# Kernel optimization log

Hardware: AMD Instinct MI355X
Metric: run time of the kernel (lower is better)

The kernel has to match this reference:

```python
import jax, jax.numpy as jnp
import numpy as np

B, D, H, DH, L = 2, 1024, 16, 64, 4
FF = 4 * D
COUNTS = (512, 256, 128, 64, 16)  # seq, local_seq, scattering, expression, fusion
EPS = 1e-5


def layer_norm(x, gamma):
    mu = jnp.mean(x, axis=-1, keepdims=True)
    var = jnp.mean((x - mu) ** 2, axis=-1, keepdims=True)
    return (x - mu) * jax.lax.rsqrt(var + EPS) * gamma


def build_zorro_mask(counts):
    # faithful to the torch code, including the `|` / `==` precedence quirk:
    # zorro_mask_fusion = (zorro_mask | tf) == FUSION(4)
    types = jnp.concatenate([jnp.full((c,), i, dtype=jnp.int32) for i, c in enumerate(counts)])
    tf, tt = types[:, None], types[None, :]
    m0 = tf == tt
    fusion_rows = (m0.astype(jnp.int32) | tf) == 4
    mask = m0 | fusion_rows
    S = int(sum(counts))
    nf = counts[4]
    exp_rows = (types == 3)[:, None]
    col_ok = (jnp.arange(S) < (S - nf))[None, :]
    return mask | (exp_rows & col_ok)


def setup_inputs() -> dict:
    key = jax.random.key(0)
    ks = jax.random.split(key, 13)
    s = 0.02
    inp = {
        "rna_tokens": jax.random.normal(ks[0], (B, COUNTS[0], D), jnp.float32),
        "roi_tokens": jax.random.normal(ks[1], (B, COUNTS[1], D), jnp.float32),
        "structure_tokens": jax.random.normal(ks[2], (B, COUNTS[2], D), jnp.float32),
        "expression_tokens": jax.random.normal(ks[3], (B, COUNTS[3], D), jnp.float32),
        "fusion_tokens": jax.random.normal(ks[4], (B, COUNTS[4], D), jnp.float32),
        "qw": jax.random.normal(ks[5], (L, D, H * DH), jnp.float32) * s,
        "kvw": jax.random.normal(ks[6], (L, D, 2 * H * DH), jnp.float32) * s,
        "ow": jax.random.normal(ks[7], (L, H * DH, D), jnp.float32) * s,
        "ag": jnp.ones((L, D), jnp.float32),
        "fg": jnp.ones((L, D), jnp.float32),
        "w1": jax.random.normal(ks[8], (L, D, FF), jnp.float32) * s,
        "w2": jax.random.normal(ks[9], (L, FF, D), jnp.float32) * s,
        "gamma": jnp.ones((D,), jnp.float32),
    }
    return inp


def reference(rna_tokens, roi_tokens, structure_tokens, expression_tokens, fusion_tokens,
              qw, kvw, ow, ag, fg, w1, w2, gamma):
    streams = (rna_tokens, roi_tokens, structure_tokens, expression_tokens, fusion_tokens)
    counts = tuple(t.shape[1] for t in streams)
    tokens = jnp.concatenate(streams, axis=1)  # [B, S, D]
    b, S, d = tokens.shape
    mask = build_zorro_mask(counts)  # [S, S] bool
    scale = DH ** -0.5
    neg = jnp.finfo(tokens.dtype).min
    attn_list = []
    for l in range(L):
        x = layer_norm(tokens, ag[l])
        q = (x @ qw[l]).reshape(b, S, H, DH)
        kv = x @ kvw[l]
        k = kv[..., : H * DH].reshape(b, S, H, DH)
        v = kv[..., H * DH:].reshape(b, S, H, DH)
        sim = jnp.einsum('bihd,bjhd->bhij', q, k) * scale
        sim = jnp.where(mask, sim, neg)
        attn = jax.nn.softmax(sim, axis=-1)  # [B, H, S, S]
        attn_list.append(attn)
        out = jnp.einsum('bhij,bjhd->bihd', attn, v).reshape(b, S, H * DH) @ ow[l]
        tokens = out + tokens
        y = layer_norm(tokens, fg[l])
        tokens = jax.nn.gelu(y @ w1[l], approximate=False) @ w2[l] + tokens
    tokens = layer_norm(tokens, gamma)
    splits = np.cumsum(counts)[:-1].tolist()
    seq_t, local_t, scat_t, exp_t, fus_t = jnp.split(tokens, splits, axis=1)
    return (seq_t, local_t, scat_t, exp_t, fus_t, jnp.stack(attn_list))
```

## Files before the change

kernel.cpp:

```cpp
#include <hip/hip_runtime.h>
#include <math.h>
#include <stdint.h>

typedef __bf16 bf16;
typedef __attribute__((ext_vector_type(8))) bf16 bf16x8;
typedef __attribute__((ext_vector_type(4))) bf16 bf16x4;
typedef __attribute__((ext_vector_type(4))) float f4;

__device__ __forceinline__ f4 mfma(bf16x8 a, bf16x8 b, f4 c){
  return __builtin_amdgcn_mfma_f32_16x16x32_bf16(a, b, c, 0, 0, 0);
}

static constexpr int S_TOT = 976;
static constexpr int MR = 1952;
static constexpr int MRP = 2048;
static constexpr size_t ATT_BASE = 1998848;
static constexpr size_t ATT_L = 30482432;

__device__ __forceinline__ void gload16(const void* g, const void* l){
  __builtin_amdgcn_global_load_lds(
      (const __attribute__((address_space(1))) void*)(uintptr_t)g,
      (__attribute__((address_space(3))) void*)(uint32_t)(uintptr_t)l,
      16, 0, 0);
}

__device__ __forceinline__ unsigned pk2(float a, float b){
  unsigned short ua = __builtin_bit_cast(unsigned short, (bf16)a);
  unsigned short ub = __builtin_bit_cast(unsigned short, (bf16)b);
  return ((unsigned)ub << 16) | (unsigned)ua;
}

__global__ __launch_bounds__(256) void k_concat_ln(const float* __restrict__ r0, const float* __restrict__ r1,
                                                   const float* __restrict__ r2, const float* __restrict__ r3,
                                                   const float* __restrict__ r4, const float* __restrict__ g,
                                                   float* __restrict__ tok, bf16* __restrict__ xb){
  int wid = threadIdx.x >> 6, lane = threadIdx.x & 63;
  int row = blockIdx.x*4 + wid;
  int b = row / S_TOT, s = row % S_TOT;
  const float* src; int off;
  if (s < 512)      { src = r0; off = b*512 + s; }
  else if (s < 768) { src = r1; off = b*256 + (s-512); }
  else if (s < 896) { src = r2; off = b*128 + (s-768); }
  else if (s < 960) { src = r3; off = b*64  + (s-896); }
  else              { src = r4; off = b*16  + (s-960); }
  const f4* p = (const f4*)src + (size_t)off*256;
  f4 v[4];
  float sum=0.f, sq=0.f;
#pragma unroll
  for (int i=0;i<4;i++){
    v[i] = p[i*64 + lane];
    ((f4*)(tok + (size_t)row*1024))[i*64 + lane] = v[i];
#pragma unroll
    for (int c=0;c<4;c++){ float x=v[i][c]; sum+=x; sq+=x*x; }
  }
#pragma unroll
  for (int d=1; d<64; d<<=1){ sum += __shfl_xor(sum,d); sq += __shfl_xor(sq,d); }
  float mu = sum*(1.f/1024.f);
  float var = sq*(1.f/1024.f) - mu*mu;
  float rs = rsqrtf(var + 1e-5f);
#pragma unroll
  for (int i=0;i<4;i++){
    f4 gg = ((const f4*)g)[i*64 + lane];
    bf16x4 o;
#pragma unroll
    for (int c=0;c<4;c++) o[c] = (bf16)((v[i][c]-mu)*rs*gg[c]);
    *(bf16x4*)&xb[(size_t)row*1024 + (size_t)(i*64+lane)*4] = o;
  }
}

__global__ __launch_bounds__(256) void k_ln_bf(const float* __restrict__ in, const float* __restrict__ g,
                                               bf16* __restrict__ out){
  int wid = threadIdx.x >> 6, lane = threadIdx.x & 63;
  int row = blockIdx.x*4 + wid;
  const float* p = in + (size_t)row*1024;
  f4 v[4];
#pragma unroll
  for (int i=0;i<4;i++) v[i] = ((const f4*)p)[i*64 + lane];
  float sum=0.f, sq=0.f;
#pragma unroll
  for (int i=0;i<4;i++){
#pragma unroll
    for (int c=0;c<4;c++){ float x=v[i][c]; sum+=x; sq+=x*x; } }
#pragma unroll
  for (int d=1; d<64; d<<=1){ sum += __shfl_xor(sum,d); sq += __shfl_xor(sq,d); }
  float mu = sum*(1.f/1024.f);
  float var = sq*(1.f/1024.f) - mu*mu;
  float rs = rsqrtf(var + 1e-5f);
#pragma unroll
  for (int i=0;i<4;i++){
    f4 gg = ((const f4*)g)[i*64 + lane];
    bf16x4 o;
#pragma unroll
    for (int c=0;c<4;c++) o[c] = (bf16)((v[i][c]-mu)*rs*gg[c]);
    *(bf16x4*)&out[(size_t)row*1024 + (size_t)(i*64+lane)*4] = o;
  }
}

template<bool LN>
__global__ __launch_bounds__(256) void k_red_ln(const float* __restrict__ pA, float* __restrict__ tokens,
                                                const float* __restrict__ g, bf16* __restrict__ xb){
  int wid = threadIdx.x >> 6, lane = threadIdx.x & 63;
  int row = blockIdx.x*4 + wid;
  const float* p0 = pA + (size_t)row*1024;
  const float* p1 = pA + (size_t)MRP*1024 + (size_t)row*1024;
  float* tp = tokens + (size_t)row*1024;
  f4 v[4];
  float sum=0.f, sq=0.f;
#pragma unroll
  for (int i=0;i<4;i++){
    f4 a = ((const f4*)p0)[i*64 + lane];
    f4 b = ((const f4*)p1)[i*64 + lane];
    f4 t = ((const f4*)tp)[i*64 + lane];
#pragma unroll
    for (int c=0;c<4;c++){ float x = t[c] + a[c] + b[c]; v[i][c] = x; if (LN){ sum += x; sq += x*x; } }
    ((f4*)tp)[i*64 + lane] = v[i];
  }
  if (LN){
#pragma unroll
    for (int d=1; d<64; d<<=1){ sum += __shfl_xor(sum,d); sq += __shfl_xor(sq,d); }
    float mu = sum*(1.f/1024.f);
    float var = sq*(1.f/1024.f) - mu*mu;
    float rs = rsqrtf(var + 1e-5f);
#pragma unroll
    for (int i=0;i<4;i++){
      f4 gg = ((const f4*)g)[i*64 + lane];
      bf16x4 o;
#pragma unroll
      for (int c=0;c<4;c++) o[c] = (bf16)((v[i][c]-mu)*rs*gg[c]);
      *(bf16x4*)&xb[(size_t)row*1024 + (size_t)(i*64+lane)*4] = o;
    }
  }
}

__global__ __launch_bounds__(256) void k_red_ln_out(const float* __restrict__ pA, float* __restrict__ tokens,
                                                    const float* __restrict__ g, float* __restrict__ out){
  int wid = threadIdx.x >> 6, lane = threadIdx.x & 63;
  int row = blockIdx.x*4 + wid;
  int b = row / S_TOT, s = row % S_TOT;
  size_t dst;
  if (s < 512)      dst = (size_t)(b*512 + s)*1024;
  else if (s < 768) dst = 1048576 + (size_t)(b*256 + (s-512))*1024;
  else if (s < 896) dst = 1572864 + (size_t)(b*128 + (s-768))*1024;
  else if (s < 960) dst = 1835008 + (size_t)(b*64  + (s-896))*1024;
  else              dst = 1966080 + (size_t)(b*16  + (s-960))*1024;
  const float* p0 = pA + (size_t)row*1024;
  const float* p1 = pA + (size_t)MRP*1024 + (size_t)row*1024;
  const float* tp = tokens + (size_t)row*1024;
  f4 v[4];
  float sum=0.f, sq=0.f;
#pragma unroll
  for (int i=0;i<4;i++){
    f4 a = ((const f4*)p0)[i*64 + lane];
    f4 bb = ((const f4*)p1)[i*64 + lane];
    f4 t = ((const f4*)tp)[i*64 + lane];
#pragma unroll
    for (int c=0;c<4;c++){ float x = t[c] + a[c] + bb[c]; v[i][c] = x; sum += x; sq += x*x; }
  }
#pragma unroll
  for (int d=1; d<64; d<<=1){ sum += __shfl_xor(sum,d); sq += __shfl_xor(sq,d); }
  float mu = sum*(1.f/1024.f);
  float var = sq*(1.f/1024.f) - mu*mu;
  float rs = rsqrtf(var + 1e-5f);
#pragma unroll
  for (int i=0;i<4;i++){
    f4 gg = ((const f4*)g)[i*64 + lane];
    f4 o;
#pragma unroll
    for (int c=0;c<4;c++) o[c] = (v[i][c]-mu)*rs*gg[c];
    ((f4*)(out + dst))[i*64 + lane] = o;
  }
}

__global__ __launch_bounds__(256) void k_wtransz(const float* __restrict__ src, int ldsrc, int coloff, long srcZ,
                                                 bf16* __restrict__ dst, int K, long dstZ){
  src += (size_t)blockIdx.z*srcZ;
  dst += (size_t)blockIdx.z*dstZ;
  __shared__ float t[32][33];
  int kb = blockIdx.x*32, nb = blockIdx.y*32;
  int tx = threadIdx.x & 31, ty = threadIdx.x >> 5;
#pragma unroll
  for (int i=0;i<32;i+=8) t[ty+i][tx] = src[(size_t)(kb+ty+i)*ldsrc + coloff + nb + tx];
  __syncthreads();
#pragma unroll
  for (int i=0;i<32;i+=8) dst[(size_t)(nb+ty+i)*K + kb + tx] = (bf16)t[tx][ty+i];
}

__global__ __launch_bounds__(256) void k_attn_pv(const bf16* __restrict__ q, const bf16* __restrict__ k,
                                                 const bf16* __restrict__ vT, int ld,
                                                 float* __restrict__ aout, bf16* __restrict__ O){
  int z = blockIdx.y; int b = z >> 4, h = z & 15;
  int wid = threadIdx.x >> 6, lane = threadIdx.x & 63;
  int r0 = (blockIdx.x*4 + wid)*16;
  if (r0 >= S_TOT) return;
  int cs, ce;
  if (r0 < 512)      { cs = 0;   ce = 512; }
  else if (r0 < 768) { cs = 512; ce = 768; }
  else if (r0 < 896) { cs = 768; ce = 896; }
  else if (r0 < 960) { cs = 0;   ce = 960; }
  else               { cs = 0;   ce = 976; }
  int lm = lane & 15, lg = lane >> 4;
  const float scale = 0.125f;
  const bf16* qp = q + (size_t)(b*S_TOT + r0 + lm)*ld + h*64 + lg*8;
  bf16x8 qf0 = *(const bf16x8*)qp;
  bf16x8 qf1 = *(const bf16x8*)(qp + 32);
  const bf16* kbase = k + (size_t)b*S_TOT*ld + h*64 + lg*8;
  const bf16* vbase = vT + (size_t)z*64*S_TOT;
  int nfull = (ce - cs) & ~31;
  bool tail = ((ce - cs) & 16) != 0;
  float s = 0.f;
  for (int cb = cs; cb < cs + nfull; cb += 32){
    const bf16* kp = kbase + (size_t)(cb + lm)*ld;
    bf16x8 k00 = *(const bf16x8*)kp;
    bf16x8 k01 = *(const bf16x8*)(kp + 32);
    const bf16* kp2 = kp + (size_t)16*ld;
    bf16x8 k10 = *(const bf16x8*)kp2;
    bf16x8 k11 = *(const bf16x8*)(kp2 + 32);
    f4 c0 = {0.f,0.f,0.f,0.f}, c1 = {0.f,0.f,0.f,0.f};
    __builtin_amdgcn_s_setprio(1);
    c0 = mfma(k00, qf0, c0); c0 = mfma(k01, qf1, c0);
    c1 = mfma(k10, qf0, c1); c1 = mfma(k11, qf1, c1);
    __builtin_amdgcn_s_setprio(0);
#pragma unroll
    for (int r=0;r<4;r++) s += __expf(c0[r]*scale) + __expf(c1[r]*scale);
  }
  if (tail){
    int cb = cs + nfull;
    const bf16* kp = kbase + (size_t)(cb + lm)*ld;
    bf16x8 k00 = *(const bf16x8*)kp;
    bf16x8 k01 = *(const bf16x8*)(kp + 32);
    f4 c0 = {0.f,0.f,0.f,0.f};
    c0 = mfma(k00, qf0, c0); c0 = mfma(k01, qf1, c0);
#pragma unroll
    for (int r=0;r<4;r++) s += __expf(c0[r]*scale);
  }
  s += __shfl_xor(s, 16);
  s += __shfl_xor(s, 32);
  float inv = 1.f / s;
  float* orow = aout + (size_t)z*S_TOT*S_TOT + (size_t)(r0 + lm)*S_TOT;
  f4 acc[4];
#pragma unroll
  for (int nf=0;nf<4;nf++){ f4 zf = {0.f,0.f,0.f,0.f}; acc[nf] = zf; }
  bool msel = (lg >= 2);
  int srcA = lm + ((lg & 1) << 5);
  int srcB = srcA + 16;
  auto step = [&](int cb, bool has2){
    const bf16* kp = kbase + (size_t)(cb + lm)*ld;
    bf16x8 k00 = *(const bf16x8*)kp;
    bf16x8 k01 = *(const bf16x8*)(kp + 32);
    f4 c0 = {0.f,0.f,0.f,0.f}, c1 = {0.f,0.f,0.f,0.f};
    __builtin_amdgcn_s_setprio(1);
    c0 = mfma(k00, qf0, c0); c0 = mfma(k01, qf1, c0);
    if (has2){
      const bf16* kp2 = kp + (size_t)16*ld;
      bf16x8 k10 = *(const bf16x8*)kp2;
      bf16x8 k11 = *(const bf16x8*)(kp2 + 32);
      c1 = mfma(k10, qf0, c1); c1 = mfma(k11, qf1, c1);
    }
    __builtin_amdgcn_s_setprio(0);
    f4 p0, p1;
#pragma unroll
    for (int r=0;r<4;r++) p0[r] = __expf(c0[r]*scale)*inv;
#pragma unroll
    for (int r=0;r<4;r++) p1[r] = has2 ? __expf(c1[r]*scale)*inv : 0.f;
    *(f4*)(orow + cb + lg*4) = p0;
    if (has2) *(f4*)(orow + cb + 16 + lg*4) = p1;
    unsigned lo0 = pk2(p0[0], p0[1]), hi0 = pk2(p0[2], p0[3]);
    unsigned lo1 = pk2(p1[0], p1[1]), hi1 = pk2(p1[2], p1[3]);
    unsigned a0 = __shfl(lo0, srcA), a1 = __shfl(lo1, srcA);
    unsigned b0 = __shfl(hi0, srcA), b1 = __shfl(hi1, srcA);
    unsigned c0s = __shfl(lo0, srcB), c1s = __shfl(lo1, srcB);
    unsigned d0 = __shfl(hi0, srcB), d1 = __shfl(hi1, srcB);
    union { unsigned u[4]; bf16x8 v; } pu;
    pu.u[0] = msel ? a1 : a0;
    pu.u[1] = msel ? b1 : b0;
    pu.u[2] = msel ? c1s : c0s;
    pu.u[3] = msel ? d1 : d0;
    bf16x8 pa = pu.v;
    __builtin_amdgcn_s_setprio(1);
#pragma unroll
    for (int nf=0;nf<4;nf++){
      bf16x8 vf = *(const bf16x8*)(vbase + (size_t)(nf*16 + lm)*S_TOT + cb + lg*8);
      acc[nf] = mfma(pa, vf, acc[nf]);
    }
    __builtin_amdgcn_s_setprio(0);
  };
  for (int cb = cs; cb < cs + nfull; cb += 32) step(cb, true);
  if (tail) step(cs + nfull, false);
  bf16* obase = O + (size_t)(b*S_TOT + r0)*1024 + h*64;
#pragma unroll
  for (int nf=0;nf<4;nf++)
#pragma unroll
    for (int r=0;r<4;r++)
      obase[(size_t)(lg*4 + r)*1024 + nf*16 + lm] = (bf16)acc[nf][r];
  float* zrow = aout + (size_t)z*S_TOT*S_TOT + (size_t)r0*S_TOT;
  int cs4 = cs >> 2, ce4 = ce >> 2;
  for (int r2=0;r2<16;r2++){
    f4* rb = (f4*)(zrow + (size_t)r2*S_TOT);
    f4 zf = {0.f,0.f,0.f,0.f};
    for (int c4 = lane; c4 < cs4; c4 += 64)        rb[c4] = zf;
    for (int c4 = ce4 + lane; c4 < 244; c4 += 64)  rb[c4] = zf;
  }
}

template<int BM, bool OUTBF, bool RESID, bool GELU, bool VT>
__global__ __launch_bounds__(256) void k_gemm2(
    const bf16* __restrict__ A, int lda,
    const bf16* __restrict__ Bw, int ldb,
    float* __restrict__ Cf, bf16* __restrict__ Cb, int ldc,
    const float* __restrict__ R, bf16* __restrict__ vTout,
    int M, int N, int K, int kz, long cz)
{
  constexpr int MF = BM/32;
  __shared__ bf16 As[2][BM*32];
  __shared__ bf16 Bs[2][128*32];
  int tid = threadIdx.x, lane = tid & 63, wid = tid >> 6;
  int lm = lane & 15, lg = lane >> 4;
  int wr = (wid >> 1)*(BM/2), wc = (wid & 1)*64;
  int mb = blockIdx.x*BM, nb = blockIdx.y*128;
  int bz = blockIdx.z;
  f4 acc[MF][4];
#pragma unroll
  for (int i=0;i<MF;i++)
#pragma unroll
    for (int j=0;j<4;j++){ f4 zf = {0.f,0.f,0.f,0.f}; acc[i][j] = zf; }
  const bf16* Ab = A + (size_t)mb*lda + (size_t)bz*kz;
  const bf16* Bb = Bw + (size_t)nb*ldb + (size_t)bz*kz;
  auto stage = [&](int kt, int buf){
    int k0 = kt*32;
#pragma unroll
    for (int it=0; it<BM/64; it++){
      int cb = it*256 + wid*64;
      int c  = cb + lane;
      gload16(Ab + (size_t)(c>>2)*lda + k0 + (c&3)*8, (char*)As[buf] + cb*16);
    }
#pragma unroll
    for (int it=0; it<2; it++){
      int cb = it*256 + wid*64;
      int c  = cb + lane;
      gload16(Bb + (size_t)(c>>2)*ldb + k0 + (c&3)*8, (char*)Bs[buf] + cb*16);
    }
  };
  stage(0, 0);
  __syncthreads();
  int nkt = K/32;
  for (int kt=0; kt<nkt; kt++){
    int cur = kt & 1;
    if (kt+1 < nkt) stage(kt+1, cur^1);
    bf16x8 af[MF], bfr[4];
#pragma unroll
    for (int mf=0; mf<MF; mf++) af[mf] = *(bf16x8*)&As[cur][(wr + mf*16 + lm)*32 + lg*8];
#pragma unroll
    for (int nf=0; nf<4; nf++)  bfr[nf] = *(bf16x8*)&Bs[cur][(wc + nf*16 + lm)*32 + lg*8];
#pragma unroll
    for (int mf=0; mf<MF; mf++)
#pragma unroll
      for (int nf=0; nf<4; nf++)
        acc[mf][nf] = mfma(af[mf], bfr[nf], acc[mf][nf]);
    __syncthreads();
  }
#pragma unroll
  for (int mf=0; mf<MF; mf++)
#pragma unroll
    for (int nf=0; nf<4; nf++)
#pragma unroll
      for (int r=0; r<4; r++){
        int row = mb + wr + mf*16 + lg*4 + r;
        if (row < M){
          int col = nb + wc + nf*16 + lm;
          float vv = acc[mf][nf][r];
          if (RESID) vv += R[(size_t)row*ldc + col];
          if (GELU){
            float u2 = vv*(1.5957691216f + 0.0713548162f*vv*vv);
            float e = __expf(u2);
            vv = vv - vv/(e + 1.f);
          }
          if (OUTBF) Cb[(size_t)row*ldc + col] = (bf16)vv;
          else       Cf[(size_t)bz*cz + (size_t)row*ldc + col] = vv;
        }
      }
  if constexpr (VT){
    if (nb >= 2048){
      __shared__ __align__(16) bf16 Ts[128][72];
#pragma unroll
      for (int hb=0; hb<2; hb++){
        __syncthreads();
        if ((wid >> 1) == hb){
#pragma unroll
          for (int mf=0; mf<MF; mf++)
#pragma unroll
            for (int nf=0; nf<4; nf++)
#pragma unroll
              for (int r=0; r<4; r++)
                Ts[wc + nf*16 + lm][mf*16 + lg*4 + r] = (bf16)acc[mf][nf][r];
        }
        __syncthreads();
        int dc = tid >> 1;
        int rh = (tid & 1)*32;
#pragma unroll
        for (int j=0;j<4;j++){
          int lr = rh + j*8;
          int srow = mb + hb*64 + lr;
          if (srow < MR){
            int bb = srow >= S_TOT;
            int ss = srow - bb*S_TOT;
            int gn = nb - 2048 + dc;
            bf16x8 d = *(bf16x8*)&Ts[dc][lr];
            *(bf16x8*)&vTout[((size_t)(bb*16 + (gn>>6))*64 + (gn&63))*S_TOT + ss] = d;
          }
        }
      }
    }
  }
}

extern "C" void kernel_launch(void* const* d_in, const int* in_sizes, int n_in,
                              void* d_out, int out_size, void* d_ws, size_t ws_size,
                              hipStream_t stream) {
  const float* rna  = (const float*)d_in[0];
  const float* roi  = (const float*)d_in[1];
  const float* stru = (const float*)d_in[2];
  const float* expr = (const float*)d_in[3];
  const float* fus  = (const float*)d_in[4];
  const float* qw   = (const float*)d_in[5];
  const float* kvw  = (const float*)d_in[6];
  const float* ow   = (const float*)d_in[7];
  const float* ag   = (const float*)d_in[8];
  const float* fg   = (const float*)d_in[9];
  const float* w1   = (const float*)d_in[10];
  const float* w2   = (const float*)d_in[11];
  const float* gamma= (const float*)d_in[12];
  float* out = (float*)d_out;

  char* wsb = (char*)d_ws;
  size_t off = 0;
  auto alc = [&](size_t n)->char*{ char* p = wsb + off; off = (off + n + 255) & ~(size_t)255; return p; };
  float* tokens = (float*)alc((size_t)MRP*1024*4);
  float* pA    = (float*)alc((size_t)2*MRP*1024*4);
  bf16* xb    = (bf16*)alc((size_t)MRP*1024*2);
  bf16* qkv   = (bf16*)alc((size_t)MRP*3072*2);
  bf16* vT    = (bf16*)alc((size_t)32*64*S_TOT*2);
  bf16* attno = (bf16*)alc((size_t)MRP*1024*2);
  bf16* hb    = (bf16*)alc((size_t)MRP*4096*2);
  bf16* wqkvT = (bf16*)alc((size_t)4*3072*1024*2);
  bf16* woT   = (bf16*)alc((size_t)4*1024*1024*2);
  bf16* w1T   = (bf16*)alc((size_t)4*4096*1024*2);
  bf16* w2T   = (bf16*)alc((size_t)4*4096*1024*2);
  if (off > ws_size) return;

  k_wtransz<<<dim3(32,32,4),  256, 0, stream>>>(qw,  1024, 0,    1048576, wqkvT,             1024, 3145728);
  k_wtransz<<<dim3(32,32,4),  256, 0, stream>>>(kvw, 2048, 0,    2097152, wqkvT + 1024*1024, 1024, 3145728);
  k_wtransz<<<dim3(32,32,4),  256, 0, stream>>>(kvw, 2048, 1024, 2097152, wqkvT + 2048*1024, 1024, 3145728);
  k_wtransz<<<dim3(32,32,4),  256, 0, stream>>>(ow,  1024, 0,    1048576, woT, 1024, 1048576);
  k_wtransz<<<dim3(32,128,4), 256, 0, stream>>>(w1,  4096, 0,    4194304, w1T, 1024, 4194304);
  k_wtransz<<<dim3(128,32,4), 256, 0, stream>>>(w2,  1024, 0,    4194304, w2T, 4096, 4194304);

  k_concat_ln<<<MR/4, 256, 0, stream>>>(rna, roi, stru, expr, fus, ag, tokens, xb);

  for (int l=0; l<4; l++){
    k_gemm2<128,true,false,false,true><<<dim3(16,24), 256, 0, stream>>>(
        xb, 1024, wqkvT + (size_t)l*3145728, 1024, nullptr, qkv, 3072, nullptr, vT, MR, 3072, 1024, 0, 0);

    float* attL = out + ATT_BASE + (size_t)l*ATT_L;
    k_attn_pv<<<dim3(16,32), 256, 0, stream>>>(qkv, qkv + 1024, vT, 3072, attL, attno);

    k_gemm2<64,false,true,false,false><<<dim3(31,8), 256, 0, stream>>>(
        attno, 1024, woT + (size_t)l*1048576, 1024, tokens, nullptr, 1024, tokens, nullptr, MR, 1024, 1024, 0, 0);

    k_ln_bf<<<MR/4, 256, 0, stream>>>(tokens, fg + l*1024, xb);

    k_gemm2<128,true,false,true,false><<<dim3(16,32), 256, 0, stream>>>(
        xb, 1024, w1T + (size_t)l*4194304, 1024, nullptr, hb, 4096, nullptr, nullptr, MR, 4096, 1024, 0, 0);

    k_gemm2<128,false,false,false,false><<<dim3(16,8,2), 256, 0, stream>>>(
        hb, 4096, w2T + (size_t)l*4194304, 4096, pA, nullptr, 1024, nullptr, nullptr, MR, 1024, 2048,
        2048, (long)MRP*1024);

    if (l < 3) k_red_ln<true><<<MR/4, 256, 0, stream>>>(pA, tokens, ag + (l+1)*1024, xb);
    else       k_red_ln_out<<<MR/4, 256, 0, stream>>>(pA, tokens, gamma, out);
  }
}
```

Baseline: 1.022 ms.

## Switch GEMM to 32x32x16 MFMA and swizzle block order for XCD locality

The GEMM kernel now uses the 32x32x16 bf16 MFMA instruction instead of 16x16x32. This halves the LDS fragment loads per MFMA and should raise matrix-core throughput. Both the GEMM and attention kernels also remap the linear block index so that consecutive blocks land on chiplets in groups of eight, which aims to improve L2 reuse across XCDs. The remap assumes the grid size is divisible by 8; if it is not, some tiles could be skipped or duplicated.

```diff
diff --git a/kernel.cpp b/kernel.cpp
--- a/kernel.cpp
+++ b/kernel.cpp
@@ -6,9 +6,13 @@
 typedef __attribute__((ext_vector_type(8))) bf16 bf16x8;
 typedef __attribute__((ext_vector_type(4))) bf16 bf16x4;
 typedef __attribute__((ext_vector_type(4))) float f4;
+typedef __attribute__((ext_vector_type(16))) float f16v;
 
 __device__ __forceinline__ f4 mfma(bf16x8 a, bf16x8 b, f4 c){
   return __builtin_amdgcn_mfma_f32_16x16x32_bf16(a, b, c, 0, 0, 0);
+}
+__device__ __forceinline__ f16v mfma32(bf16x8 a, bf16x8 b, f16v c){
+  return __builtin_amdgcn_mfma_f32_32x32x16_bf16(a, b, c, 0, 0, 0);
 }
 
 static constexpr int S_TOT = 976;
@@ -188,9 +192,14 @@
 __global__ __launch_bounds__(256) void k_attn_pv(const bf16* __restrict__ q, const bf16* __restrict__ k,
                                                  const bf16* __restrict__ vT, int ld,
                                                  float* __restrict__ aout, bf16* __restrict__ O){
-  int z = blockIdx.y; int b = z >> 4, h = z & 15;
+  int nxy = gridDim.x * gridDim.y;
+  int lin0 = blockIdx.y * gridDim.x + blockIdx.x;
+  int lin = (lin0 & 7)*(nxy >> 3) + (lin0 >> 3);
+  int bxs = lin % gridDim.x;
+  int z = lin / gridDim.x;
+  int b = z >> 4, h = z & 15;
   int wid = threadIdx.x >> 6, lane = threadIdx.x & 63;
-  int r0 = (blockIdx.x*4 + wid)*16;
+  int r0 = (bxs*4 + wid)*16;
   if (r0 >= S_TOT) return;
   int cs, ce;
   if (r0 < 512)      { cs = 0;   ce = 512; }
@@ -310,19 +319,24 @@
     const float* __restrict__ R, bf16* __restrict__ vTout,
     int M, int N, int K, int kz, long cz)
 {
-  constexpr int MF = BM/32;
+  constexpr int MI = BM/64;
   __shared__ bf16 As[2][BM*32];
   __shared__ bf16 Bs[2][128*32];
   int tid = threadIdx.x, lane = tid & 63, wid = tid >> 6;
-  int lm = lane & 15, lg = lane >> 4;
+  int l31 = lane & 31, kh = lane >> 5;
   int wr = (wid >> 1)*(BM/2), wc = (wid & 1)*64;
-  int mb = blockIdx.x*BM, nb = blockIdx.y*128;
+  int nxy = gridDim.x * gridDim.y;
+  int lin0 = blockIdx.y * gridDim.x + blockIdx.x;
+  int lin = (lin0 & 7)*(nxy >> 3) + (lin0 >> 3);
+  int mb = (lin % gridDim.x)*BM, nb = (lin / gridDim.x)*128;
   int bz = blockIdx.z;
-  f4 acc[MF][4];
-#pragma unroll
-  for (int i=0;i<MF;i++)
-#pragma unroll
-    for (int j=0;j<4;j++){ f4 zf = {0.f,0.f,0.f,0.f}; acc[i][j] = zf; }
+  f16v acc[MI][2];
+#pragma unroll
+  for (int i=0;i<MI;i++)
+#pragma unroll
+    for (int j=0;j<2;j++)
+#pragma unroll
+      for (int e=0;e<16;e++) acc[i][j][e] = 0.f;
   const bf16* Ab = A + (size_t)mb*lda + (size_t)bz*kz;
   const bf16* Bb = Bw + (size_t)nb*ldb + (size_t)bz*kz;
   auto stage = [&](int kt, int buf){
@@ -346,28 +360,36 @@
   for (int kt=0; kt<nkt; kt++){
     int cur = kt & 1;
     if (kt+1 < nkt) stage(kt+1, cur^1);
-    bf16x8 af[MF], bfr[4];
-#pragma unroll
-    for (int mf=0; mf<MF; mf++) af[mf] = *(bf16x8*)&As[cur][(wr + mf*16 + lm)*32 + lg*8];
-#pragma unroll
-    for (int nf=0; nf<4; nf++)  bfr[nf] = *(bf16x8*)&Bs[cur][(wc + nf*16 + lm)*32 + lg*8];
-#pragma unroll
-    for (int mf=0; mf<MF; mf++)
-#pragma unroll
-      for (int nf=0; nf<4; nf++)
-        acc[mf][nf] = mfma(af[mf], bfr[nf], acc[mf][nf]);
+    bf16x8 af[MI][2], bfr[2][2];
+#pragma unroll
+    for (int mi=0; mi<MI; mi++)
+#pragma unroll
+      for (int ks=0; ks<2; ks++)
+        af[mi][ks] = *(bf16x8*)&As[cur][(wr + mi*32 + l31)*32 + ks*16 + kh*8];
+#pragma unroll
+    for (int ni=0; ni<2; ni++)
+#pragma unroll
+      for (int ks=0; ks<2; ks++)
+        bfr[ni][ks] = *(bf16x8*)&Bs[cur][(wc + ni*32 + l31)*32 + ks*16 + kh*8];
+#pragma unroll
+    for (int mi=0; mi<MI; mi++)
+#pragma unroll
+      for (int ni=0; ni<2; ni++)
+#pragma unroll
+        for (int ks=0; ks<2; ks++)
+          acc[mi][ni] = mfma32(af[mi][ks], bfr[ni][ks], acc[mi][ni]);
     __syncthreads();
   }
 #pragma unroll
-  for (int mf=0; mf<MF; mf++)
-#pragma unroll
-    for (int nf=0; nf<4; nf++)
-#pragma unroll
-      for (int r=0; r<4; r++){
-        int row = mb + wr + mf*16 + lg*4 + r;
+  for (int mi=0; mi<MI; mi++)
+#pragma unroll
+    for (int ni=0; ni<2; ni++){
+      int col = nb + wc + ni*32 + l31;
+#pragma unroll
+      for (int reg=0; reg<16; reg++){
+        int row = mb + wr + mi*32 + (reg&3) + 8*(reg>>2) + 4*kh;
         if (row < M){
-          int col = nb + wc + nf*16 + lm;
-          float vv = acc[mf][nf][r];
+          float vv = acc[mi][ni][reg];
           if (RESID) vv += R[(size_t)row*ldc + col];
           if (GELU){
             float u2 = vv*(1.5957691216f + 0.0713548162f*vv*vv);
@@ -378,6 +400,7 @@
           else       Cf[(size_t)bz*cz + (size_t)row*ldc + col] = vv;
         }
       }
+    }
   if constexpr (VT){
     if (nb >= 2048){
       __shared__ __align__(16) bf16 Ts[128][72];
@@ -386,12 +409,12 @@
         __syncthreads();
         if ((wid >> 1) == hb){
 #pragma unroll
-          for (int mf=0; mf<MF; mf++)
-#pragma unroll
-            for (int nf=0; nf<4; nf++)
-#pragma unroll
-              for (int r=0; r<4; r++)
-                Ts[wc + nf*16 + lm][mf*16 + lg*4 + r] = (bf16)acc[mf][nf][r];
+          for (int mi=0; mi<MI; mi++)
+#pragma unroll
+            for (int ni=0; ni<2; ni++)
+#pragma unroll
+              for (int reg=0; reg<16; reg++)
+                Ts[wc + ni*32 + l31][mi*32 + (reg&3) + 8*(reg>>2) + 4*kh] = (bf16)acc[mi][ni][reg];
         }
         __syncthreads();
         int dc = tid >> 1;
```

Result: slower. 1.054 ms (+3.2%).

## Merge weight transposes into one launch and hoist attention mask zeroing

Applied to the files above, without the earlier changes.

Replaces the six weight-transpose launches with a single kernel that decodes which matrix and tile each block handles. It also moves the zero-fill of masked attention-probability entries out of the per-layer attention kernel into one upfront kernel covering all four layers, using 256 threads per block. This is meant to cut launch overhead and take the zero-store tail off the attention kernel's critical path. The cost is one large separate zero-fill pass over the attention output at the start.

```diff
diff --git a/kernel.cpp b/kernel.cpp
--- a/kernel.cpp
+++ b/kernel.cpp
@@ -28,6 +28,29 @@
   unsigned short ua = __builtin_bit_cast(unsigned short, (bf16)a);
   unsigned short ub = __builtin_bit_cast(unsigned short, (bf16)b);
   return ((unsigned)ub << 16) | (unsigned)ua;
+}
+
+__device__ __forceinline__ void mask_span(int r0, int& cs, int& ce){
+  if (r0 < 512)      { cs = 0;   ce = 512; }
+  else if (r0 < 768) { cs = 512; ce = 768; }
+  else if (r0 < 896) { cs = 768; ce = 896; }
+  else if (r0 < 960) { cs = 0;   ce = 960; }
+  else               { cs = 0;   ce = 976; }
+}
+
+__global__ __launch_bounds__(256) void k_zero_mask(float* __restrict__ aout){
+  int z = blockIdx.y;
+  int r0 = blockIdx.x*16;
+  float* base = aout + (size_t)blockIdx.z*ATT_L + (size_t)z*S_TOT*S_TOT;
+  int cs, ce; mask_span(r0, cs, ce);
+  int cs4 = cs >> 2, ce4 = ce >> 2;
+  f4 zf = {0.f,0.f,0.f,0.f};
+#pragma unroll
+  for (int r2=0;r2<16;r2++){
+    f4* rb = (f4*)(base + (size_t)(r0 + r2)*S_TOT);
+    for (int c4 = threadIdx.x; c4 < cs4; c4 += 256)        rb[c4] = zf;
+    for (int c4 = ce4 + threadIdx.x; c4 < 244; c4 += 256)  rb[c4] = zf;
+  }
 }
 
 __global__ __launch_bounds__(256) void k_concat_ln(const float* __restrict__ r0, const float* __restrict__ r1,
@@ -171,18 +194,43 @@
   }
 }
 
-__global__ __launch_bounds__(256) void k_wtransz(const float* __restrict__ src, int ldsrc, int coloff, long srcZ,
-                                                 bf16* __restrict__ dst, int K, long dstZ){
-  src += (size_t)blockIdx.z*srcZ;
-  dst += (size_t)blockIdx.z*dstZ;
-  __shared__ float t[32][33];
-  int kb = blockIdx.x*32, nb = blockIdx.y*32;
+__global__ __launch_bounds__(256) void k_wtrans_all(const float* __restrict__ qw, const float* __restrict__ kvw,
+                                                    const float* __restrict__ ow, const float* __restrict__ w1,
+                                                    const float* __restrict__ w2,
+                                                    bf16* __restrict__ wqkvT, bf16* __restrict__ woT,
+                                                    bf16* __restrict__ w1T, bf16* __restrict__ w2T){
+  int t = blockIdx.x;
+  int l = t / 12288; t -= l*12288;
+  const float* src; bf16* dst; int ldsrc, K, coloff, kb, nb;
+  if (t < 3072){
+    int c = t >> 10, tt = t & 1023;
+    kb = (tt & 31)*32; nb = (tt >> 5)*32;
+    if (c == 0){ src = qw + (size_t)l*1048576; ldsrc = 1024; coloff = 0; }
+    else       { src = kvw + (size_t)l*2097152; ldsrc = 2048; coloff = (c==2)?1024:0; }
+    dst = wqkvT + (size_t)l*3145728 + (size_t)c*1048576; K = 1024;
+  } else if (t < 4096){
+    int tt = t - 3072;
+    kb = (tt & 31)*32; nb = (tt >> 5)*32;
+    src = ow + (size_t)l*1048576; ldsrc = 1024; coloff = 0;
+    dst = woT + (size_t)l*1048576; K = 1024;
+  } else if (t < 8192){
+    int tt = t - 4096;
+    kb = (tt & 31)*32; nb = (tt >> 5)*32;
+    src = w1 + (size_t)l*4194304; ldsrc = 4096; coloff = 0;
+    dst = w1T + (size_t)l*4194304; K = 1024;
+  } else {
+    int tt = t - 8192;
+    kb = (tt & 127)*32; nb = (tt >> 7)*32;
+    src = w2 + (size_t)l*4194304; ldsrc = 1024; coloff = 0;
+    dst = w2T + (size_t)l*4194304; K = 4096;
+  }
+  __shared__ float tbuf[32][33];
   int tx = threadIdx.x & 31, ty = threadIdx.x >> 5;
 #pragma unroll
-  for (int i=0;i<32;i+=8) t[ty+i][tx] = src[(size_t)(kb+ty+i)*ldsrc + coloff + nb + tx];
+  for (int i=0;i<32;i+=8) tbuf[ty+i][tx] = src[(size_t)(kb+ty+i)*ldsrc + coloff + nb + tx];
   __syncthreads();
 #pragma unroll
-  for (int i=0;i<32;i+=8) dst[(size_t)(nb+ty+i)*K + kb + tx] = (bf16)t[tx][ty+i];
+  for (int i=0;i<32;i+=8) dst[(size_t)(nb+ty+i)*K + kb + tx] = (bf16)tbuf[tx][ty+i];
 }
 
 __global__ __launch_bounds__(256) void k_attn_pv(const bf16* __restrict__ q, const bf16* __restrict__ k,
@@ -192,12 +240,7 @@
   int wid = threadIdx.x >> 6, lane = threadIdx.x & 63;
   int r0 = (blockIdx.x*4 + wid)*16;
   if (r0 >= S_TOT) return;
-  int cs, ce;
-  if (r0 < 512)      { cs = 0;   ce = 512; }
-  else if (r0 < 768) { cs = 512; ce = 768; }
-  else if (r0 < 896) { cs = 768; ce = 896; }
-  else if (r0 < 960) { cs = 0;   ce = 960; }
-  else               { cs = 0;   ce = 976; }
+  int cs, ce; mask_span(r0, cs, ce);
   int lm = lane & 15, lg = lane >> 4;
   const float scale = 0.125f;
   const bf16* qp = q + (size_t)(b*S_TOT + r0 + lm)*ld + h*64 + lg*8;
@@ -292,14 +335,6 @@
 #pragma unroll
     for (int r=0;r<4;r++)
       obase[(size_t)(lg*4 + r)*1024 + nf*16 + lm] = (bf16)acc[nf][r];
-  float* zrow = aout + (size_t)z*S_TOT*S_TOT + (size_t)r0*S_TOT;
-  int cs4 = cs >> 2, ce4 = ce >> 2;
-  for (int r2=0;r2<16;r2++){
-    f4* rb = (f4*)(zrow + (size_t)r2*S_TOT);
-    f4 zf = {0.f,0.f,0.f,0.f};
-    for (int c4 = lane; c4 < cs4; c4 += 64)        rb[c4] = zf;
-    for (int c4 = ce4 + lane; c4 < 244; c4 += 64)  rb[c4] = zf;
-  }
 }
 
 template<int BM, bool OUTBF, bool RESID, bool GELU, bool VT>
@@ -447,12 +482,9 @@
   bf16* w2T   = (bf16*)alc((size_t)4*4096*1024*2);
   if (off > ws_size) return;
 
-  k_wtransz<<<dim3(32,32,4),  256, 0, stream>>>(qw,  1024, 0,    1048576, wqkvT,             1024, 3145728);
-  k_wtransz<<<dim3(32,32,4),  256, 0, stream>>>(kvw, 2048, 0,    2097152, wqkvT + 1024*1024, 1024, 3145728);
-  k_wtransz<<<dim3(32,32,4),  256, 0, stream>>>(kvw, 2048, 1024, 2097152, wqkvT + 2048*1024, 1024, 3145728);
-  k_wtransz<<<dim3(32,32,4),  256, 0, stream>>>(ow,  1024, 0,    1048576, woT, 1024, 1048576);
-  k_wtransz<<<dim3(32,128,4), 256, 0, stream>>>(w1,  4096, 0,    4194304, w1T, 1024, 4194304);
-  k_wtransz<<<dim3(128,32,4), 256, 0, stream>>>(w2,  1024, 0,    4194304, w2T, 4096, 4194304);
+  k_zero_mask<<<dim3(61,32,4), 256, 0, stream>>>(out + ATT_BASE);
+
+  k_wtrans_all<<<4*12288, 256, 0, stream>>>(qw, kvw, ow, w1, w2, wqkvT, woT, w1T, w2T);
 
   k_concat_ln<<<MR/4, 256, 0, stream>>>(rna, roi, stru, expr, fus, ag, tokens, xb);
 
```

Result: slower. 1.057 ms (+3.5%).
